# Kernel optimization log

Measured on AMD Instinct MI355X. Metric: run time of the kernel, lower is better.

Reference implementation:

```python
import jax, jax.numpy as jnp
import numpy as np

ACOUSTIC_BOOKS = [1, 2, 3, 4, 5, 6, 7, 8, 9, 10, 11, 12, 13, 14, 15, 16, 17, 17, 17, 17, 17]


def setup_inputs() -> dict:
    key = jax.random.key(0)
    ks = jax.random.split(key, 6)
    B, C, T, D, K, NB = 4, 512, 4096, 256, 2048, 18
    return {
        "x": jax.random.normal(ks[0], (B, C, T), dtype=jnp.float32),
        "Win_s": jax.random.normal(ks[1], (D, C), dtype=jnp.float32) * 0.05,
        "Win_a": jax.random.normal(ks[2], (D, C), dtype=jnp.float32) * 0.05,
        "Wout_s": jax.random.normal(ks[3], (C, D), dtype=jnp.float32) * 0.05,
        "Wout_a": jax.random.normal(ks[4], (C, D), dtype=jnp.float32) * 0.05,
        "E": jax.random.normal(ks[5], (NB, K, D), dtype=jnp.float32),
    }


def _nearest(z, e):
    # z: [B, D, T], e: [K, D] -> codes [B, T] via argmin of squared euclidean dist
    zt = z.transpose(0, 2, 1)  # [B, T, D]
    d2 = (jnp.sum(zt * zt, axis=-1, keepdims=True)
          - 2.0 * jnp.einsum('btd,kd->btk', zt, e)
          + jnp.sum(e * e, axis=-1))  # [B, T, K]
    return jnp.argmin(d2, axis=-1)  # [B, T]


def reference(x, Win_s, Win_a, Wout_s, Wout_a, E):
    # ---- encode ----
    xs = jnp.einsum('dc,bct->bdt', Win_s, x)  # in_proj_s (1x1 conv, no bias)
    codes = [_nearest(xs, E[0])]
    xa = jnp.einsum('dc,bct->bdt', Win_a, x)  # in_proj_a
    for cb in ACOUSTIC_BOOKS:
        idx = _nearest(xa, E[cb])
        xa = xa - E[cb][idx].transpose(0, 2, 1)  # residual subtract (decode gather)
        codes.append(idx)
    codes = jnp.stack(codes, axis=1)  # [B, 22, T]

    # ---- decode ----
    semantic = E[0][codes[:, 0]].transpose(0, 2, 1)  # [B, D, T]
    acoustic = jnp.zeros_like(semantic)
    for i, cb in enumerate(ACOUSTIC_BOOKS):
        acoustic = acoustic + E[cb][codes[:, i + 1]].transpose(0, 2, 1)
    out = (jnp.einsum('cd,bdt->bct', Wout_s, semantic)
           + jnp.einsum('cd,bdt->bct', Wout_a, acoustic))  # [B, 512, T]
    return out, codes
```

## Files before the change

### kernel.cpp

```cpp
#include <hip/hip_runtime.h>
#include <float.h>

#define TT 4096
#define BB 4
#define CC 512
#define DD 256
#define KK 2048
#define MM (BB*TT)
#define NBOOKS 22
#define EPS_PAIR 0.5f
#define EPS_FULL 0.5f
#define ZSTR 260
#define ASTR 264
#define RPB 32

typedef _Float16 half8_t __attribute__((ext_vector_type(8)));
typedef float f32x4 __attribute__((ext_vector_type(4)));

__device__ __forceinline__ uint32_t packsc(float s, int code) {
  uint32_t b = __float_as_uint(s);
  uint32_t key = b ^ ((uint32_t)((int32_t)b >> 31) | 0x80000000u);
  return (key & 0xFFFFF800u) | (uint32_t)code;
}
__device__ __forceinline__ float unpacksc(uint32_t p) {
  uint32_t key = p & 0xFFFFF800u;
  uint32_t b = (key & 0x80000000u) ? (key ^ 0x80000000u) : ~key;
  return __uint_as_float(b);
}
__device__ __forceinline__ void ins4(uint32_t& v1, uint32_t& v2, uint32_t& v3,
                                     uint32_t& v4, uint32_t p) {
  uint32_t t1 = max(v1, p);  v1 = min(v1, p);
  uint32_t t2 = max(v2, t1); v2 = min(v2, t1);
  uint32_t t3 = max(v3, t2); v3 = min(v3, t2);
  v4 = min(v4, t3);
}

__global__ __launch_bounds__(256) void proj_kernel(const float* __restrict__ x,
    const float* __restrict__ Ws, const float* __restrict__ Wa,
    float* __restrict__ xs, float* __restrict__ xa)
{
  __shared__ float xt[16*64];
  __shared__ float wsl[16*68];
  __shared__ float wal[16*68];
  const int tid = threadIdx.x;
  const int t0 = blockIdx.x*64, d0 = blockIdx.y*64, b = blockIdx.z;
  const int u = tid & 63, cq = tid >> 6;
  const int tx = tid & 15, ty = tid >> 4;
  const float* xb = x + (size_t)b*CC*TT;
  float accS[4][4] = {{0}}, accA[4][4] = {{0}};
  for (int c0 = 0; c0 < CC; c0 += 16) {
    __syncthreads();
    #pragma unroll
    for (int i = 0; i < 4; ++i) {
      int cc = cq*4 + i;
      xt[cc*64 + u] = xb[(size_t)(c0+cc)*TT + t0 + u];
    }
    {
      float4 wv = *(const float4*)&Ws[(size_t)(d0+u)*CC + c0 + cq*4];
      wsl[(cq*4+0)*68 + u] = wv.x; wsl[(cq*4+1)*68 + u] = wv.y;
      wsl[(cq*4+2)*68 + u] = wv.z; wsl[(cq*4+3)*68 + u] = wv.w;
      wv = *(const float4*)&Wa[(size_t)(d0+u)*CC + c0 + cq*4];
      wal[(cq*4+0)*68 + u] = wv.x; wal[(cq*4+1)*68 + u] = wv.y;
      wal[(cq*4+2)*68 + u] = wv.z; wal[(cq*4+3)*68 + u] = wv.w;
    }
    __syncthreads();
    #pragma unroll
    for (int cc = 0; cc < 16; ++cc) {
      float4 tq = *(const float4*)&xt[cc*64 + ty*4];
      float4 sq = *(const float4*)&wsl[cc*68 + tx*4];
      float4 aq = *(const float4*)&wal[cc*68 + tx*4];
      float tf[4] = {tq.x,tq.y,tq.z,tq.w};
      float sf[4] = {sq.x,sq.y,sq.z,sq.w};
      float af[4] = {aq.x,aq.y,aq.z,aq.w};
      #pragma unroll
      for (int i = 0; i < 4; ++i)
        #pragma unroll
        for (int j = 0; j < 4; ++j) {
          accS[i][j] = fmaf(tf[i], sf[j], accS[i][j]);
          accA[i][j] = fmaf(tf[i], af[j], accA[i][j]);
        }
    }
  }
  #pragma unroll
  for (int i = 0; i < 4; ++i) {
    size_t r = (size_t)b*TT + t0 + ty*4 + i;
    float4 o;
    o.x = accS[i][0]; o.y = accS[i][1]; o.z = accS[i][2]; o.w = accS[i][3];
    *(float4*)&xs[r*DD + d0 + tx*4] = o;
    o.x = accA[i][0]; o.y = accA[i][1]; o.z = accA[i][2]; o.w = accA[i][3];
    *(float4*)&xa[r*DD + d0 + tx*4] = o;
  }
}

__global__ __launch_bounds__(256) void e2_kernel(const float* __restrict__ E,
    float* __restrict__ e2)
{
  int gid = blockIdx.x*256 + threadIdx.x;
  int wid = gid >> 6, lane = gid & 63;
  if (wid < 18*KK) {
    float4 v = *(const float4*)&E[(size_t)wid*DD + lane*4];
    float s = v.x*v.x + v.y*v.y + v.z*v.z + v.w*v.w;
    #pragma unroll
    for (int m = 1; m <= 32; m <<= 1) s += __shfl_xor(s, m);
    if (lane == 0) e2[wid] = s;
  }
}

__global__ __launch_bounds__(256) void cvt_e16_kernel(const float* __restrict__ E,
    _Float16* __restrict__ E16)
{
  size_t i = ((size_t)blockIdx.x*256 + threadIdx.x)*8;
  float4 u = *(const float4*)&E[i];
  float4 v = *(const float4*)&E[i+4];
  half8_t h;
  h[0]=(_Float16)u.x; h[1]=(_Float16)u.y; h[2]=(_Float16)u.z; h[3]=(_Float16)u.w;
  h[4]=(_Float16)v.x; h[5]=(_Float16)v.y; h[6]=(_Float16)v.z; h[7]=(_Float16)v.w;
  *(half8_t*)&E16[i] = h;
}

__global__ __launch_bounds__(256)
void fused_encode_kernel(
    const float* __restrict__ xs_g, const float* __restrict__ xa_g,
    const float* __restrict__ E, const _Float16* __restrict__ E16,
    const float* __restrict__ e2, int* __restrict__ codes0,
    float* __restrict__ codes_f, float* __restrict__ aco_g)
{
  const int tid = threadIdx.x;
  const int lane = tid & 63, wave = tid >> 6;
  const int ln15 = lane & 15, lq = lane >> 4;
  const int row0 = blockIdx.x * RPB;

  __shared__ float Z[RPB][ZSTR];
  __shared__ _Float16 A16[RPB][ASTR];
  __shared__ uint32_t L1[4][RPB], L2[4][RPB], L3[4][RPB], L4[4][RPB];
  __shared__ int   codes_s[RPB];
  __shared__ int   flist[RPB];
  __shared__ int   cA[RPB], cB[RPB];
  __shared__ int   nfull, ncand;
  __shared__ double Rv[4];
  __shared__ int    Ri[4];

  const int ldr = tid & 31, cg = tid >> 5;
  const int sr = tid >> 3, sg = tid & 7;
  const int vr = tid >> 3, vc = (tid & 7)*32;

  for (int ib = 0; ib < NBOOKS; ++ib) {
    const int book = (ib <= 17) ? ib : 17;
    const float*     Eb   = E   + (size_t)book*KK*DD;
    const _Float16*  E16b = E16 + (size_t)book*KK*DD;
    const float*     e2b  = e2  + (size_t)book*KK;

    if (ib <= 1) {
      const float* src = (ib == 0) ? xs_g : xa_g;
      const float* sp = src + (size_t)(row0 + ldr)*DD + cg*32;
      #pragma unroll
      for (int j = 0; j < 8; ++j)
        *(float4*)&Z[ldr][cg*32 + j*4] = *(const float4*)(sp + j*4);
    }
    if (tid == 0) { nfull = 0; ncand = 0; }
    __syncthreads();

    #pragma unroll
    for (int j = 0; j < 4; ++j) {
      float4 u = *(const float4*)&Z[vr][vc + j*8];
      float4 v = *(const float4*)&Z[vr][vc + j*8 + 4];
      half8_t h;
      h[0]=(_Float16)u.x; h[1]=(_Float16)u.y; h[2]=(_Float16)u.z; h[3]=(_Float16)u.w;
      h[4]=(_Float16)v.x; h[5]=(_Float16)v.y; h[6]=(_Float16)v.z; h[7]=(_Float16)v.w;
      *(half8_t*)&A16[vr][vc + j*8] = h;
    }
    __syncthreads();

    uint32_t p1[2][4], p2[2][4], p3[2][4], p4[2][4];
    #pragma unroll
    for (int mt = 0; mt < 2; ++mt)
      #pragma unroll
      for (int j = 0; j < 4; ++j) {
        p1[mt][j] = 0xFFFFFFFFu; p2[mt][j] = 0xFFFFFFFFu;
        p3[mt][j] = 0xFFFFFFFFu; p4[mt][j] = 0xFFFFFFFFu;
      }

    const _Float16* ebase = E16b + (size_t)(wave*512 + ln15)*DD + lq*8;
    const _Float16* a0p = &A16[ln15][lq*8];
    const _Float16* a1p = &A16[16 + ln15][lq*8];

    for (int nt = 0; nt < 32; nt += 2) {
      const _Float16* bp0 = ebase + (size_t)nt*16*DD;
      const _Float16* bp1 = bp0 + 16*DD;
      half8_t B0[8];
      #pragma unroll
      for (int ks = 0; ks < 8; ++ks) B0[ks] = *(const half8_t*)(bp0 + ks*32);
      f32x4 a00 = (f32x4){0.f,0.f,0.f,0.f};
      f32x4 a01 = (f32x4){0.f,0.f,0.f,0.f};
      f32x4 a10 = (f32x4){0.f,0.f,0.f,0.f};
      f32x4 a11 = (f32x4){0.f,0.f,0.f,0.f};
      #pragma unroll
      for (int ks = 0; ks < 8; ++ks) {
        half8_t B1k = *(const half8_t*)(bp1 + ks*32);
        half8_t fa0 = *(const half8_t*)(a0p + ks*32);
        half8_t fa1 = *(const half8_t*)(a1p + ks*32);
        a00 = __builtin_amdgcn_mfma_f32_16x16x32_f16(fa0, B0[ks], a00, 0, 0, 0);
        a01 = __builtin_amdgcn_mfma_f32_16x16x32_f16(fa1, B0[ks], a01, 0, 0, 0);
        a10 = __builtin_amdgcn_mfma_f32_16x16x32_f16(fa0, B1k, a10, 0, 0, 0);
        a11 = __builtin_amdgcn_mfma_f32_16x16x32_f16(fa1, B1k, a11, 0, 0, 0);
      }
      int code0 = wave*512 + nt*16 + ln15;
      int code1 = code0 + 16;
      float e20 = e2b[code0], e21 = e2b[code1];
      #pragma unroll
      for (int j = 0; j < 4; ++j) {
        ins4(p1[0][j], p2[0][j], p3[0][j], p4[0][j], packsc(fmaf(-2.f, a00[j], e20), code0));
        ins4(p1[1][j], p2[1][j], p3[1][j], p4[1][j], packsc(fmaf(-2.f, a01[j], e20), code0));
        ins4(p1[0][j], p2[0][j], p3[0][j], p4[0][j], packsc(fmaf(-2.f, a10[j], e21), code1));
        ins4(p1[1][j], p2[1][j], p3[1][j], p4[1][j], packsc(fmaf(-2.f, a11[j], e21), code1));
      }
    }

    #pragma unroll
    for (int mt = 0; mt < 2; ++mt)
      #pragma unroll
      for (int j = 0; j < 4; ++j) {
        uint32_t v1 = p1[mt][j], v2 = p2[mt][j], v3 = p3[mt][j], v4 = p4[mt][j];
        #pragma unroll
        for (int m = 1; m <= 8; m <<= 1) {
          uint32_t w1 = (uint32_t)__shfl_xor((int)v1, m);
          uint32_t w2 = (uint32_t)__shfl_xor((int)v2, m);
          uint32_t w3 = (uint32_t)__shfl_xor((int)v3, m);
          uint32_t w4 = (uint32_t)__shfl_xor((int)v4, m);
          ins4(v1, v2, v3, v4, w1);
          ins4(v1, v2, v3, v4, w2);
          ins4(v1, v2, v3, v4, w3);
          ins4(v1, v2, v3, v4, w4);
        }
        if (ln15 == 0) {
          int rl = mt*16 + lq*4 + j;
          L1[wave][rl] = v1; L2[wave][rl] = v2;
          L3[wave][rl] = v3; L4[wave][rl] = v4;
        }
      }
    __syncthreads();
    if (tid < RPB) {
      uint32_t v1 = L1[0][tid], v2 = L2[0][tid], v3 = L3[0][tid], v4 = L4[0][tid];
      #pragma unroll
      for (int w = 1; w < 4; ++w) {
        ins4(v1, v2, v3, v4, L1[w][tid]);
        ins4(v1, v2, v3, v4, L2[w][tid]);
        ins4(v1, v2, v3, v4, L3[w][tid]);
        ins4(v1, v2, v3, v4, L4[w][tid]);
      }
      int a1 = (int)(v1 & 2047u), a2 = (int)(v2 & 2047u), a3 = (int)(v3 & 2047u);
      float f1 = unpacksc(v1), f2 = unpacksc(v2), f4 = unpacksc(v4);
      codes_s[tid] = a1;
      int rg = row0 + tid;
      codes_f[((size_t)(rg >> 12)*NBOOKS + ib)*TT + (rg & (TT-1))] = (float)a1;
      if (ib == 0) codes0[rg] = a1;
      if (f4 - f1 < EPS_FULL) {
        flist[atomicAdd(&nfull, 1)] = tid;
      } else if (f2 - f1 < EPS_PAIR) {
        int p = atomicAdd(&ncand, 1);
        cA[p] = tid | (a1 << 6) | (a2 << 17);
        cB[p] = a3;
      }
    }
    __syncthreads();

    int nfl = nfull;
    for (int f = 0; f < nfl; ++f) {
      int row = flist[f];
      double bestv = DBL_MAX; int besti = 0x7fffffff;
      #pragma unroll
      for (int q = 0; q < 8; ++q) {
        int k = q*256 + tid;
        const float* er = Eb + (size_t)k*DD;
        double s0 = 0.0, s1 = 0.0;
        for (int d = 0; d < DD; d += 8) {
          float4 e0 = *(const float4*)(er + d);
          float4 e1 = *(const float4*)(er + d + 4);
          double x0 = (double)Z[row][d+0] - (double)e0.x;
          double x1 = (double)Z[row][d+1] - (double)e0.y;
          double x2 = (double)Z[row][d+2] - (double)e0.z;
          double x3 = (double)Z[row][d+3] - (double)e0.w;
          s0 += x0*x0 + x1*x1 + x2*x2 + x3*x3;
          double x4 = (double)Z[row][d+4] - (double)e1.x;
          double x5 = (double)Z[row][d+5] - (double)e1.y;
          double x6 = (double)Z[row][d+6] - (double)e1.z;
          double x7 = (double)Z[row][d+7] - (double)e1.w;
          s1 += x4*x4 + x5*x5 + x6*x6 + x7*x7;
        }
        double s = s0 + s1;
        if (s < bestv || (s == bestv && k < besti)) { bestv = s; besti = k; }
      }
      #pragma unroll
      for (int m = 1; m <= 32; m <<= 1) {
        double ov = __shfl_xor(bestv, m);
        int    oi = __shfl_xor(besti, m);
        if (ov < bestv || (ov == bestv && oi < besti)) { bestv = ov; besti = oi; }
      }
      if (lane == 0) { Rv[wave] = bestv; Ri[wave] = besti; }
      __syncthreads();
      if (tid == 0) {
        double bvv = Rv[0]; int bii = Ri[0];
        #pragma unroll
        for (int w = 1; w < 4; ++w)
          if (Rv[w] < bvv || (Rv[w] == bvv && Ri[w] < bii)) { bvv = Rv[w]; bii = Ri[w]; }
        codes_s[row] = bii;
        int rg = row0 + row;
        codes_f[((size_t)(rg >> 12)*NBOOKS + ib)*TT + (rg & (TT-1))] = (float)bii;
        if (ib == 0) codes0[rg] = bii;
      }
      __syncthreads();
    }

    {
      int ncd = ncand;
      for (int f = wave; f < ncd; f += 4) {
        int pk = cA[f];
        int row = pk & 63;
        int cand[3];
        cand[0] = (pk >> 6) & 2047;
        cand[1] = (pk >> 17) & 2047;
        cand[2] = cB[f];
        double bv = DBL_MAX; int bi = 0x7fffffff;
        #pragma unroll
        for (int t = 0; t < 3; ++t) {
          int cc = cand[t];
          const float* er = Eb + (size_t)cc*DD + lane*4;
          const float* zr = &Z[row][lane*4];
          double d0 = (double)zr[0] - (double)er[0];
          double d1 = (double)zr[1] - (double)er[1];
          double d2 = (double)zr[2] - (double)er[2];
          double d3 = (double)zr[3] - (double)er[3];
          double s = d0*d0 + d1*d1 + d2*d2 + d3*d3;
          #pragma unroll
          for (int m = 1; m <= 32; m <<= 1) s += __shfl_xor(s, m);
          if (s < bv || (s == bv && cc < bi)) { bv = s; bi = cc; }
        }
        if (lane == 0) {
          codes_s[row] = bi;
          int rg = row0 + row;
          codes_f[((size_t)(rg >> 12)*NBOOKS + ib)*TT + (rg & (TT-1))] = (float)bi;
          if (ib == 0) codes0[rg] = bi;
        }
      }
    }
    __syncthreads();

    if (ib >= 1) {
      int code = codes_s[sr];
      const float* er = Eb + (size_t)code*DD;
      #pragma unroll
      for (int j = 0; j < 8; ++j) {
        int c = sg*4 + j*32;
        float4 e = *(const float4*)(er + c);
        float4 z = *(const float4*)&Z[sr][c];
        z.x -= e.x; z.y -= e.y; z.z -= e.z; z.w -= e.w;
        *(float4*)&Z[sr][c] = z;
      }
    }
    __syncthreads();
  }

  {
    const float* xp = xa_g + (size_t)(row0 + ldr)*DD + cg*32;
    float*       ap = aco_g + (size_t)(row0 + ldr)*DD + cg*32;
    #pragma unroll
    for (int j = 0; j < 8; ++j) {
      float4 x0 = *(const float4*)(xp + j*4);
      float4 zf = *(const float4*)&Z[ldr][cg*32 + j*4];
      float4 o;
      o.x = x0.x - zf.x; o.y = x0.y - zf.y; o.z = x0.z - zf.z; o.w = x0.w - zf.w;
      *(float4*)(ap + j*4) = o;
    }
  }
}

__global__ __launch_bounds__(256) void final_kernel(
    const float* __restrict__ Wos, const float* __restrict__ Woa,
    const float* __restrict__ E0, const int* __restrict__ codes0,
    const float* __restrict__ aco, float* __restrict__ out)
{
  __shared__ float wsl[16*68], wal[16*68], sml[16*68], acl[16*68];
  const int tid = threadIdx.x;
  const int t0 = blockIdx.x*64, c0 = blockIdx.y*64, b = blockIdx.z;
  const int u = tid & 63, dq = tid >> 6;
  const int tx = tid & 15, ty = tid >> 4;
  int code = codes0[b*TT + t0 + u];
  const float* smr = E0 + (size_t)code*DD;
  const float* acr = aco + (size_t)(b*TT + t0 + u)*DD;
  const float* wsr = Wos + (size_t)(c0+u)*DD;
  const float* war = Woa + (size_t)(c0+u)*DD;
  float accS[4][4] = {{0}}, accA[4][4] = {{0}};
  for (int dc0 = 0; dc0 < DD; dc0 += 16) {
    __syncthreads();
    float4 v;
    v = *(const float4*)(wsr + dc0 + dq*4);
    wsl[(dq*4+0)*68+u]=v.x; wsl[(dq*4+1)*68+u]=v.y; wsl[(dq*4+2)*68+u]=v.z; wsl[(dq*4+3)*68+u]=v.w;
    v = *(const float4*)(war + dc0 + dq*4);
    wal[(dq*4+0)*68+u]=v.x; wal[(dq*4+1)*68+u]=v.y; wal[(dq*4+2)*68+u]=v.z; wal[(dq*4+3)*68+u]=v.w;
    v = *(const float4*)(smr + dc0 + dq*4);
    sml[(dq*4+0)*68+u]=v.x; sml[(dq*4+1)*68+u]=v.y; sml[(dq*4+2)*68+u]=v.z; sml[(dq*4+3)*68+u]=v.w;
    v = *(const float4*)(acr + dc0 + dq*4);
    acl[(dq*4+0)*68+u]=v.x; acl[(dq*4+1)*68+u]=v.y; acl[(dq*4+2)*68+u]=v.z; acl[(dq*4+3)*68+u]=v.w;
    __syncthreads();
    #pragma unroll
    for (int d = 0; d < 16; ++d) {
      float4 cs = *(const float4*)&wsl[d*68 + tx*4];
      float4 ca = *(const float4*)&wal[d*68 + tx*4];
      float4 ts = *(const float4*)&sml[d*68 + ty*4];
      float4 ta = *(const float4*)&acl[d*68 + ty*4];
      float csf[4]={cs.x,cs.y,cs.z,cs.w}, caf[4]={ca.x,ca.y,ca.z,ca.w};
      float tsf[4]={ts.x,ts.y,ts.z,ts.w}, taf[4]={ta.x,ta.y,ta.z,ta.w};
      #pragma unroll
      for (int i = 0; i < 4; ++i)
        #pragma unroll
        for (int j = 0; j < 4; ++j) {
          accS[i][j] = fmaf(csf[i], tsf[j], accS[i][j]);
          accA[i][j] = fmaf(caf[i], taf[j], accA[i][j]);
        }
    }
  }
  size_t ob = (size_t)b*CC*TT;
  #pragma unroll
  for (int i = 0; i < 4; ++i) {
    float4 r;
    r.x = accS[i][0] + accA[i][0];
    r.y = accS[i][1] + accA[i][1];
    r.z = accS[i][2] + accA[i][2];
    r.w = accS[i][3] + accA[i][3];
    *(float4*)&out[ob + (size_t)(c0 + tx*4 + i)*TT + t0 + ty*4] = r;
  }
}

extern "C" void kernel_launch(void* const* d_in, const int* in_sizes, int n_in,
                              void* d_out, int out_size, void* d_ws, size_t ws_size,
                              hipStream_t stream) {
  const float* x    = (const float*)d_in[0];
  const float* Wins = (const float*)d_in[1];
  const float* Wina = (const float*)d_in[2];
  const float* Wos  = (const float*)d_in[3];
  const float* Woa  = (const float*)d_in[4];
  const float* E    = (const float*)d_in[5];
  float* out = (float*)d_out;
  float* codes_f = out + (size_t)BB*CC*TT;

  _Float16* E16 = (_Float16*)d_out;

  float* xs  = (float*)d_ws;
  float* xa  = xs + (size_t)MM*DD;
  float* aco = xa + (size_t)MM*DD;
  float* e2  = aco + (size_t)MM*DD;
  int* codes_i = (int*)(e2 + 18*KK);

  proj_kernel<<<dim3(TT/64, DD/64, BB), 256, 0, stream>>>(x, Wins, Wina, xs, xa);
  e2_kernel<<<(18*KK*64)/256, 256, 0, stream>>>(E, e2);
  cvt_e16_kernel<<<(18*KK*DD)/8/256, 256, 0, stream>>>(E, E16);

  fused_encode_kernel<<<MM/RPB, 256, 0, stream>>>(xs, xa, E, E16, e2,
                                                  codes_i, codes_f, aco);

  final_kernel<<<dim3(TT/64, CC/64, BB), 256, 0, stream>>>(Wos, Woa, E, codes_i, aco, out);
}
```

Measured before the change: 1.672 ms.

## Use 512 threads per block in fused encode kernel, splitting codebook across 8 waves

The fused encode block grows from 4 to 8 waves. Each wave now scans 256 codewords instead of 512, and the cross-wave top-4 merge, full-rescan and candidate loops are widened to match. Thread-to-row mappings for the load, convert, residual and output loops are rewritten for 512 threads. This halves the serial MFMA loop per block and adds more waves to hide latency, at the cost of a larger cross-wave reduction and more register/LDS pressure per block, which may reduce blocks per CU.

```diff
diff --git a/kernel.cpp b/kernel.cpp
--- a/kernel.cpp
+++ b/kernel.cpp
@@ -118,7 +118,7 @@
   *(half8_t*)&E16[i] = h;
 }
 
-__global__ __launch_bounds__(256)
+__global__ __launch_bounds__(512)
 void fused_encode_kernel(
     const float* __restrict__ xs_g, const float* __restrict__ xa_g,
     const float* __restrict__ E, const _Float16* __restrict__ E16,
@@ -132,17 +132,15 @@
 
   __shared__ float Z[RPB][ZSTR];
   __shared__ _Float16 A16[RPB][ASTR];
-  __shared__ uint32_t L1[4][RPB], L2[4][RPB], L3[4][RPB], L4[4][RPB];
+  __shared__ uint32_t L1[8][RPB], L2[8][RPB], L3[8][RPB], L4[8][RPB];
   __shared__ int   codes_s[RPB];
   __shared__ int   flist[RPB];
   __shared__ int   cA[RPB], cB[RPB];
   __shared__ int   nfull, ncand;
-  __shared__ double Rv[4];
-  __shared__ int    Ri[4];
-
-  const int ldr = tid & 31, cg = tid >> 5;
-  const int sr = tid >> 3, sg = tid & 7;
-  const int vr = tid >> 3, vc = (tid & 7)*32;
+  __shared__ double Rv[8];
+  __shared__ int    Ri[8];
+
+  const int ldr = tid >> 4, cg = tid & 15;
 
   for (int ib = 0; ib < NBOOKS; ++ib) {
     const int book = (ib <= 17) ? ib : 17;
@@ -152,22 +150,25 @@
 
     if (ib <= 1) {
       const float* src = (ib == 0) ? xs_g : xa_g;
-      const float* sp = src + (size_t)(row0 + ldr)*DD + cg*32;
-      #pragma unroll
-      for (int j = 0; j < 8; ++j)
-        *(float4*)&Z[ldr][cg*32 + j*4] = *(const float4*)(sp + j*4);
+      const float* sp = src + (size_t)(row0 + ldr)*DD;
+      #pragma unroll
+      for (int j = 0; j < 4; ++j)
+        *(float4*)&Z[ldr][cg*4 + j*64] = *(const float4*)(sp + cg*4 + j*64);
     }
     if (tid == 0) { nfull = 0; ncand = 0; }
     __syncthreads();
 
-    #pragma unroll
-    for (int j = 0; j < 4; ++j) {
-      float4 u = *(const float4*)&Z[vr][vc + j*8];
-      float4 v = *(const float4*)&Z[vr][vc + j*8 + 4];
-      half8_t h;
-      h[0]=(_Float16)u.x; h[1]=(_Float16)u.y; h[2]=(_Float16)u.z; h[3]=(_Float16)u.w;
-      h[4]=(_Float16)v.x; h[5]=(_Float16)v.y; h[6]=(_Float16)v.z; h[7]=(_Float16)v.w;
-      *(half8_t*)&A16[vr][vc + j*8] = h;
+    {
+      int vc = cg*16;
+      #pragma unroll
+      for (int j = 0; j < 2; ++j) {
+        float4 u = *(const float4*)&Z[ldr][vc + j*8];
+        float4 v = *(const float4*)&Z[ldr][vc + j*8 + 4];
+        half8_t h;
+        h[0]=(_Float16)u.x; h[1]=(_Float16)u.y; h[2]=(_Float16)u.z; h[3]=(_Float16)u.w;
+        h[4]=(_Float16)v.x; h[5]=(_Float16)v.y; h[6]=(_Float16)v.z; h[7]=(_Float16)v.w;
+        *(half8_t*)&A16[ldr][vc + j*8] = h;
+      }
     }
     __syncthreads();
 
@@ -180,11 +181,11 @@
         p3[mt][j] = 0xFFFFFFFFu; p4[mt][j] = 0xFFFFFFFFu;
       }
 
-    const _Float16* ebase = E16b + (size_t)(wave*512 + ln15)*DD + lq*8;
+    const _Float16* ebase = E16b + (size_t)(wave*256 + ln15)*DD + lq*8;
     const _Float16* a0p = &A16[ln15][lq*8];
     const _Float16* a1p = &A16[16 + ln15][lq*8];
 
-    for (int nt = 0; nt < 32; nt += 2) {
+    for (int nt = 0; nt < 16; nt += 2) {
       const _Float16* bp0 = ebase + (size_t)nt*16*DD;
       const _Float16* bp1 = bp0 + 16*DD;
       half8_t B0[8];
@@ -204,7 +205,7 @@
         a10 = __builtin_amdgcn_mfma_f32_16x16x32_f16(fa0, B1k, a10, 0, 0, 0);
         a11 = __builtin_amdgcn_mfma_f32_16x16x32_f16(fa1, B1k, a11, 0, 0, 0);
       }
-      int code0 = wave*512 + nt*16 + ln15;
+      int code0 = wave*256 + nt*16 + ln15;
       int code1 = code0 + 16;
       float e20 = e2b[code0], e21 = e2b[code1];
       #pragma unroll
@@ -242,7 +243,7 @@
     if (tid < RPB) {
       uint32_t v1 = L1[0][tid], v2 = L2[0][tid], v3 = L3[0][tid], v4 = L4[0][tid];
       #pragma unroll
-      for (int w = 1; w < 4; ++w) {
+      for (int w = 1; w < 8; ++w) {
         ins4(v1, v2, v3, v4, L1[w][tid]);
         ins4(v1, v2, v3, v4, L2[w][tid]);
         ins4(v1, v2, v3, v4, L3[w][tid]);
@@ -269,8 +270,8 @@
       int row = flist[f];
       double bestv = DBL_MAX; int besti = 0x7fffffff;
       #pragma unroll
-      for (int q = 0; q < 8; ++q) {
-        int k = q*256 + tid;
+      for (int q = 0; q < 4; ++q) {
+        int k = q*512 + tid;
         const float* er = Eb + (size_t)k*DD;
         double s0 = 0.0, s1 = 0.0;
         for (int d = 0; d < DD; d += 8) {
@@ -301,7 +302,7 @@
       if (tid == 0) {
         double bvv = Rv[0]; int bii = Ri[0];
         #pragma unroll
-        for (int w = 1; w < 4; ++w)
+        for (int w = 1; w < 8; ++w)
           if (Rv[w] < bvv || (Rv[w] == bvv && Ri[w] < bii)) { bvv = Rv[w]; bii = Ri[w]; }
         codes_s[row] = bii;
         int rg = row0 + row;
@@ -313,7 +314,7 @@
 
     {
       int ncd = ncand;
-      for (int f = wave; f < ncd; f += 4) {
+      for (int f = wave; f < ncd; f += 8) {
         int pk = cA[f];
         int row = pk & 63;
         int cand[3];
@@ -346,30 +347,31 @@
     __syncthreads();
 
     if (ib >= 1) {
-      int code = codes_s[sr];
+      int code = codes_s[ldr];
       const float* er = Eb + (size_t)code*DD;
       #pragma unroll
-      for (int j = 0; j < 8; ++j) {
-        int c = sg*4 + j*32;
+      for (int j = 0; j < 4; ++j) {
+        int c = cg*4 + j*64;
         float4 e = *(const float4*)(er + c);
-        float4 z = *(const float4*)&Z[sr][c];
+        float4 z = *(const float4*)&Z[ldr][c];
         z.x -= e.x; z.y -= e.y; z.z -= e.z; z.w -= e.w;
-        *(float4*)&Z[sr][c] = z;
+        *(float4*)&Z[ldr][c] = z;
       }
     }
     __syncthreads();
   }
 
   {
-    const float* xp = xa_g + (size_t)(row0 + ldr)*DD + cg*32;
-    float*       ap = aco_g + (size_t)(row0 + ldr)*DD + cg*32;
-    #pragma unroll
-    for (int j = 0; j < 8; ++j) {
-      float4 x0 = *(const float4*)(xp + j*4);
-      float4 zf = *(const float4*)&Z[ldr][cg*32 + j*4];
+    const float* xp = xa_g + (size_t)(row0 + ldr)*DD;
+    float*       ap = aco_g + (size_t)(row0 + ldr)*DD;
+    #pragma unroll
+    for (int j = 0; j < 4; ++j) {
+      int c = cg*4 + j*64;
+      float4 x0 = *(const float4*)(xp + c);
+      float4 zf = *(const float4*)&Z[ldr][c];
       float4 o;
       o.x = x0.x - zf.x; o.y = x0.y - zf.y; o.z = x0.z - zf.z; o.w = x0.w - zf.w;
-      *(float4*)(ap + j*4) = o;
+      *(float4*)(ap + c) = o;
     }
   }
 }
@@ -455,7 +457,7 @@
   e2_kernel<<<(18*KK*64)/256, 256, 0, stream>>>(E, e2);
   cvt_e16_kernel<<<(18*KK*DD)/8/256, 256, 0, stream>>>(E, E16);
 
-  fused_encode_kernel<<<MM/RPB, 256, 0, stream>>>(xs, xa, E, E16, e2,
+  fused_encode_kernel<<<MM/RPB, 512, 0, stream>>>(xs, xa, E, E16, e2,
                                                   codes_i, codes_f, aco);
 
   final_kernel<<<dim3(TT/64, CC/64, BB), 256, 0, stream>>>(Wos, Woa, E, codes_i, aco, out);
```

New measurement: 2.091 ms. 25.0% more time.
